# Optimization experiments

Measured on AMD Instinct MI355X. Metric: run time of the kernel, lower is better.

## Reference

```python
import jax, jax.numpy as jnp
import numpy as np

CDIM = 32
SCALES = (1, 16, 64, 256, 1024, 4096)  # last entry == T
INV_TEMP = 100.0
ENT_W = 0.1
COMMIT_W = 0.2
Q_SCALE = 1.0 / float(np.sqrt(CDIM))


def _interp_area(x, pt):
    # x: [B, T, C] -> [B, pt, C]; T divisible by pt so 'area' == block mean
    B, T, C = x.shape
    return x.reshape(B, pt, T // pt, C).mean(axis=2)


def _interp_linear(x, T):
    # x: [B, pt, C] -> [B, T, C]; mode='linear', align_corners=False
    pt = x.shape[1]
    pos = (jnp.arange(T, dtype=jnp.float32) + 0.5) * (pt / T) - 0.5
    pos = jnp.clip(pos, 0.0, pt - 1.0)
    lo = jnp.floor(pos).astype(jnp.int32)
    hi = jnp.minimum(lo + 1, pt - 1)
    w = (pos - lo.astype(jnp.float32))[None, :, None]
    return x[:, lo] * (1.0 - w) + x[:, hi] * w


def _bsq(f):
    # L2 normalize (torch F.normalize: clamp_min on norm)
    f = f / jnp.maximum(jnp.linalg.norm(f, axis=-1, keepdims=True), 1e-12)
    # sign quantize with STE
    zhat = jnp.where(f > 0, Q_SCALE, -Q_SCALE).astype(f.dtype)
    quantized = f + jax.lax.stop_gradient(zhat - f)
    # soft entropy loss
    p = jax.nn.sigmoid(-4.0 * f * (INV_TEMP / float(np.sqrt(CDIM))))
    prob = jnp.stack([p, 1.0 - p], axis=-1)  # [B, T, C, 2]
    ent = lambda c: -(c * jnp.log(c + 1e-8)).sum(axis=-1)
    per_sample_entropy = ent(prob).sum(axis=-1).mean()
    avg_prob = prob.mean(axis=(0, 1))  # [C, 2]
    cb_entropy = ent(avg_prob).sum()
    entropy_penalty = (per_sample_entropy - cb_entropy) / INV_TEMP
    commit = ((jax.lax.stop_gradient(quantized) - f) ** 2).sum(axis=-1).mean()
    aux = entropy_penalty * ENT_W + commit * COMMIT_W
    bits = (quantized > 0).astype(jnp.int32)
    return quantized, bits, aux


def setup_inputs() -> dict:
    key = jax.random.key(0)
    B, T, C = 128, SCALES[-1], CDIM
    return {"f_BTC": jax.random.normal(key, (B, T, C), dtype=jnp.float32)}


def reference(f_BTC):
    B, T, C = f_BTC.shape
    quantized_out = jnp.zeros_like(f_BTC)
    residual = f_BTC
    losses, bit_list = [], []
    for pt in SCALES:
        interp_res = _interp_area(residual, pt) if pt != T else residual
        q, bits, loss = _bsq(interp_res)
        q = _interp_linear(q, T) if pt != T else q
        residual = residual - jax.lax.stop_gradient(q)
        quantized_out = quantized_out + q
        bit_list.append(bits)
        losses.append(loss)
    all_losses = jnp.stack(losses, axis=-1)       # [num_scales]
    all_bits = jnp.concatenate(bit_list, axis=1)  # [B, sum(SCALES), C]
    return quantized_out, all_bits, all_losses
```

## Files before the change

kernel.cpp:

```cpp
#include <hip/hip_runtime.h>
#include <hip/hip_bf16.h>
#include <cstddef>
#include <cstdint>

#define NB 128
#define NT 4096
#define NC 32
#define BITROWS 5457
#define QV_ROWS 1361
#define QOUT_ELEMS (NB*NT*NC)
#define BITS_ELEMS (NB*BITROWS*NC)

#define ACC_OFF  22298624

__device__ __constant__ float kQSC = 0.17677669529663687f;
__device__ __constant__ float kSIG = 17.67766952966369f;

__device__ __forceinline__ float interp_eval(const float* __restrict__ q, int P, int t, int c) {
  float pos = ((float)t + 0.5f) * ((float)P * (1.0f / 4096.0f)) - 0.5f;
  pos = fminf(fmaxf(pos, 0.0f), (float)(P - 1));
  const int lo = (int)pos;
  const int hi = min(lo + 1, P - 1);
  const float w = pos - (float)lo;
  const float a = __fmul_rn(q[lo * NC + c], 1.0f - w);
  const float b = __fmul_rn(q[hi * NC + c], w);
  return __fadd_rn(a, b);
}

__device__ __forceinline__ float interp_slice(const float* __restrict__ q, int P, int base, int t, int c) {
  float pos = ((float)t + 0.5f) * ((float)P * (1.0f / 4096.0f)) - 0.5f;
  pos = fminf(fmaxf(pos, 0.0f), (float)(P - 1));
  const int lo = (int)pos;
  const int hi = min(lo + 1, P - 1);
  const float w = pos - (float)lo;
  const float a = __fmul_rn(q[(lo - base) * NC + c], 1.0f - w);
  const float b = __fmul_rn(q[(hi - base) * NC + c], w);
  return __fadd_rn(a, b);
}

__device__ __forceinline__ void process_elem(
    float msum, float invn, int b, int rowOff, int j, int c,
    float* qlsRow, float* __restrict__ qvG, float* __restrict__ bitsG,
    float& entA, float& comA, float& pA)
{
  const float m = msum * invn;
  float ss = m * m;
  #pragma unroll
  for (int mk = 16; mk; mk >>= 1) ss += __shfl_xor(ss, mk, 32);
  const float den = fmaxf(sqrtf(ss), 1e-12f);
  const float fn = m / den;
  const bool bit = fn > 0.0f;
  const float zh = bit ? kQSC : -kQSC;
  const float qvv = fn + (zh - fn);
  if (qlsRow) qlsRow[c] = qvv;
  if (qvG) qvG[(size_t)b * (QV_ROWS * NC) + (size_t)(rowOff + j) * NC + c] = qvv;
  bitsG[(size_t)b * (BITROWS * NC) + (size_t)(rowOff + j) * NC + c] = bit ? 1.0f : 0.0f;
  const float arg = (-4.0f * fn) * kSIG;
  const float p = 1.0f / (1.0f + __expf(-arg));
  const float ent = -(p * __logf(p + 1e-8f) + (1.0f - p) * __logf((1.0f - p) + 1e-8f));
  const float d = qvv - fn;
  entA += ent; comA += d * d; pA += p;
}

__device__ __forceinline__ void reduce_losses(
    int sIdx, float entA, float comA, float pA, int tid, int nWaves,
    double* __restrict__ acc, float* redE, float* redC, float* redP)
{
  float e = entA, cm = comA;
  #pragma unroll
  for (int mk = 32; mk; mk >>= 1) { e += __shfl_xor(e, mk, 64); cm += __shfl_xor(cm, mk, 64); }
  const float p = pA + __shfl_xor(pA, 32, 64);
  const int w = tid >> 6, lane = tid & 63;
  if (lane == 0) { redE[w] = e; redC[w] = cm; }
  if (lane < 32) redP[w * 32 + lane] = p;
  __syncthreads();
  if (tid == 0) {
    double te = 0.0, tc = 0.0;
    for (int i = 0; i < nWaves; ++i) { te += (double)redE[i]; tc += (double)redC[i]; }
    atomicAdd(&acc[sIdx], te);
    atomicAdd(&acc[6 + sIdx], tc);
  }
  if (tid < 32) {
    float tp = 0.0f;
    for (int i = 0; i < nWaves; ++i) tp += redP[i * 32 + tid];
    atomicAdd(&acc[12 + sIdx * 32 + tid], (double)tp);
  }
  __syncthreads();
}

__global__ __launch_bounds__(1024) void k_coarse(
    const float* __restrict__ f, float* __restrict__ qv,
    float* __restrict__ bitsOut, double* __restrict__ acc)
{
  __shared__ float S[256 * NC];
  __shared__ float qls[81 * NC];
  __shared__ float red[1024];
  __shared__ float redE[16], redC[16], redP[16 * 32];
  const int b = blockIdx.x, tid = threadIdx.x;
  const int c = tid & 31;

  for (int e = tid; e < 256 * NC; e += 1024) {
    const int cc = e & 31;
    const int j = e >> 5;
    const float* p = f + (size_t)b * (NT * NC) + (size_t)j * 16 * NC + cc;
    float s = 0.0f;
    #pragma unroll
    for (int k = 0; k < 16; ++k) s += p[k * NC];
    S[e] = s;
  }
  __syncthreads();

  float entA, comA, pA;

  entA = comA = pA = 0.0f;
  {
    const int g = tid >> 5;
    float part = 0.0f;
    #pragma unroll
    for (int j = 0; j < 8; ++j) part += S[(g * 8 + j) * NC + c];
    red[tid] = part;
  }
  __syncthreads();
  if (tid < 32) {
    float msum = 0.0f;
    for (int g = 0; g < 32; ++g) msum += red[g * 32 + tid];
    process_elem(msum, 1.0f / 4096.0f, b, 0, 0, tid, &qls[0], qv, bitsOut, entA, comA, pA);
  }
  reduce_losses(0, entA, comA, pA, tid, 16, acc, redE, redC, redP);
  {
    const float corr = 16.0f * qls[c];
    for (int e = tid; e < 8192; e += 1024) S[e] -= corr;
  }
  __syncthreads();

  entA = comA = pA = 0.0f;
  if (tid < 512) {
    const int j = tid >> 5;
    float msum = 0.0f;
    for (int jj = 0; jj < 16; ++jj) msum += S[(j * 16 + jj) * NC + c];
    process_elem(msum, 1.0f / 256.0f, b, 1, j, c, &qls[(1 + j) * NC], qv, bitsOut, entA, comA, pA);
  }
  reduce_losses(1, entA, comA, pA, tid, 16, acc, redE, redC, redP);
  for (int e = tid; e < 8192; e += 1024) {
    const int jj = e >> 5;
    float cs = 0.0f;
    #pragma unroll
    for (int k = 0; k < 16; ++k) cs += interp_eval(&qls[1 * NC], 16, jj * 16 + k, c);
    S[e] -= cs;
  }
  __syncthreads();

  entA = comA = pA = 0.0f;
  for (int out = tid; out < 2048; out += 1024) {
    const int j = out >> 5;
    float msum = 0.0f;
    #pragma unroll
    for (int jj = 0; jj < 4; ++jj) msum += S[(j * 4 + jj) * NC + c];
    process_elem(msum, 1.0f / 64.0f, b, 17, j, c, &qls[(17 + j) * NC], qv, bitsOut, entA, comA, pA);
  }
  reduce_losses(2, entA, comA, pA, tid, 16, acc, redE, redC, redP);
  for (int e = tid; e < 8192; e += 1024) {
    const int jj = e >> 5;
    float cs = 0.0f;
    #pragma unroll
    for (int k = 0; k < 16; ++k) cs += interp_eval(&qls[17 * NC], 64, jj * 16 + k, c);
    S[e] -= cs;
  }
  __syncthreads();

  entA = comA = pA = 0.0f;
  for (int out = tid; out < 8192; out += 1024) {
    const int j = out >> 5;
    process_elem(S[out], 1.0f / 16.0f, b, 81, j, c, nullptr, qv, bitsOut, entA, comA, pA);
  }
  reduce_losses(3, entA, comA, pA, tid, 16, acc, redE, redC, redP);
}

__global__ __launch_bounds__(256) void k_s45(
    const float* __restrict__ f, const float* __restrict__ qv,
    float* __restrict__ qout, float* __restrict__ bitsOut, double* __restrict__ acc)
{
  __shared__ float ql0[NC];
  __shared__ float ql1[3 * NC];
  __shared__ float ql2[6 * NC];
  __shared__ float ql3[18 * NC];
  __shared__ float ql4[66 * NC];
  __shared__ float redE[4], redC[4], redP[4 * 32];
  const int b = blockIdx.x >> 4, seg = blockIdx.x & 15;
  const int tid = threadIdx.x, c = tid & 31, rloc = tid >> 5;
  const int t0 = seg * 256;
  const float* __restrict__ qb = qv + (size_t)b * (QV_ROWS * NC);
  const float* __restrict__ fb = f + (size_t)b * (NT * NC);
  const int b1 = seg - 1, b2 = 4 * seg - 1, b3 = 16 * seg - 1, b4 = 64 * seg - 1;
  if (tid < NC) ql0[tid] = qb[tid];
  for (int e = tid; e < 3 * NC; e += 256) {
    const int r = min(max(b1 + (e >> 5), 0), 15);
    ql1[e] = qb[(1 + r) * NC + (e & 31)];
  }
  for (int e = tid; e < 6 * NC; e += 256) {
    const int r = min(max(b2 + (e >> 5), 0), 63);
    ql2[e] = qb[(17 + r) * NC + (e & 31)];
  }
  for (int e = tid; e < 18 * NC; e += 256) {
    const int r = min(max(b3 + (e >> 5), 0), 255);
    ql3[e] = qb[(81 + r) * NC + (e & 31)];
  }
  __syncthreads();

  float entA = 0.0f, comA = 0.0f, pA = 0.0f;
  for (int pass = 0; pass < 8; ++pass) {
    const int i = seg * 64 + pass * 8 + rloc;
    const float* fp = fb + (size_t)i * 4 * NC + c;
    float msum = 0.0f;
    #pragma unroll
    for (int k = 0; k < 4; ++k) {
      const int t = i * 4 + k;
      float r = fp[k * NC];
      r -= ql0[c];
      r -= interp_slice(ql1, 16,  b1, t, c);
      r -= interp_slice(ql2, 64,  b2, t, c);
      r -= interp_slice(ql3, 256, b3, t, c);
      msum += r;
    }
    process_elem(msum, 0.25f, b, 337, i, c,
                 &ql4[(size_t)(i - b4) * NC], nullptr, bitsOut, entA, comA, pA);
  }
  {
    int hr = -1;
    if (rloc == 0 && seg > 0)       hr = 64 * seg - 1;
    else if (rloc == 1 && seg < 15) hr = 64 * seg + 64;
    if (hr >= 0) {
      const float* fp = fb + (size_t)hr * 4 * NC + c;
      float msum = 0.0f;
      #pragma unroll
      for (int k = 0; k < 4; ++k) {
        const int t = hr * 4 + k;
        float r = fp[k * NC];
        r -= ql0[c];
        r -= interp_slice(ql1, 16,  b1, t, c);
        r -= interp_slice(ql2, 64,  b2, t, c);
        r -= interp_slice(ql3, 256, b3, t, c);
        msum += r;
      }
      const float m = msum * 0.25f;
      float ss = m * m;
      #pragma unroll
      for (int mk = 16; mk; mk >>= 1) ss += __shfl_xor(ss, mk, 32);
      const float den = fmaxf(sqrtf(ss), 1e-12f);
      const float fn = m / den;
      const float zh = (fn > 0.0f) ? kQSC : -kQSC;
      ql4[(size_t)(hr - b4) * NC + c] = fn + (zh - fn);
    }
  }
  reduce_losses(4, entA, comA, pA, tid, 4, acc, redE, redC, redP);

  entA = 0.0f; comA = 0.0f; pA = 0.0f;
  for (int pass = 0; pass < 32; ++pass) {
    const int t = t0 + pass * 8 + rloc;
    const float fv = fb[(size_t)t * NC + c];
    const float q0 = ql0[c];
    const float q1 = interp_slice(ql1, 16,   b1, t, c);
    const float q2 = interp_slice(ql2, 64,   b2, t, c);
    const float q3 = interp_slice(ql3, 256,  b3, t, c);
    const float q4 = interp_slice(ql4, 1024, b4, t, c);
    float r = fv;
    r -= q0; r -= q1; r -= q2; r -= q3; r -= q4;
    float qs = q0; qs += q1; qs += q2; qs += q3; qs += q4;
    float ss = r * r;
    #pragma unroll
    for (int mk = 16; mk; mk >>= 1) ss += __shfl_xor(ss, mk, 32);
    const float den = fmaxf(sqrtf(ss), 1e-12f);
    const float fn = r / den;
    const bool bit = fn > 0.0f;
    const float zh = bit ? kQSC : -kQSC;
    const float qvv = fn + (zh - fn);
    qout[(size_t)b * (NT * NC) + (size_t)t * NC + c] = qs + qvv;
    bitsOut[(size_t)b * (BITROWS * NC) + (size_t)(1361 + t) * NC + c] = bit ? 1.0f : 0.0f;
    const float arg = (-4.0f * fn) * kSIG;
    const float p = 1.0f / (1.0f + __expf(-arg));
    entA += -(p * __logf(p + 1e-8f) + (1.0f - p) * __logf((1.0f - p) + 1e-8f));
    const float d = qvv - fn;
    comA += d * d;
    pA += p;
  }
  reduce_losses(5, entA, comA, pA, tid, 4, acc, redE, redC, redP);
}

__global__ void k_losses(const double* __restrict__ acc, float* __restrict__ out) {
  const int s = threadIdx.x;
  if (s >= 6) return;
  const int pts[6] = {1, 16, 64, 256, 1024, 4096};
  const double n = 128.0 * (double)pts[s];
  const double pse = acc[s] / n;
  const double commit = acc[6 + s] / n;
  double cbe = 0.0;
  for (int c = 0; c < 32; ++c) {
    const double ap = acc[12 + s * 32 + c] / n;
    cbe += -(ap * log(ap + 1e-8) + (1.0 - ap) * log((1.0 - ap) + 1e-8));
  }
  const double pen = (pse - cbe) / 100.0;
  out[s] = (float)(pen * 0.1 + commit * 0.2);
}

extern "C" void kernel_launch(void* const* d_in, const int* in_sizes, int n_in,
                              void* d_out, int out_size, void* d_ws, size_t ws_size,
                              hipStream_t stream) {
  const float* f = (const float*)d_in[0];
  float* qout = (float*)d_out;
  float* bitsOut = qout + QOUT_ELEMS;
  float* lossesOut = qout + (QOUT_ELEMS + BITS_ELEMS);
  float* qv = (float*)d_ws;
  double* acc = (double*)((char*)d_ws + ACC_OFF);

  hipMemsetAsync(acc, 0, 204 * sizeof(double), stream);
  k_coarse<<<NB, 1024, 0, stream>>>(f, qv, bitsOut, acc);
  k_s45<<<NB * 16, 256, 0, stream>>>(f, qv, qout, bitsOut, acc);
  k_losses<<<1, 64, 0, stream>>>(acc, lossesOut);
}
```

Measured before the change: 335.0 us.

## Split coarse-scale kernel into parallel block-sum, scale-0 and two-segment coarse kernels

The single per-batch coarse kernel (128 blocks) is split into three kernels. A grid-wide kernel computes the 16-row block sums into workspace, a small kernel handles scale 0, and a two-segment-per-batch kernel handles scales 1-3 using halo rows that are recomputed redundantly for the interpolation. The goal is to raise parallelism beyond 128 blocks on a many-CU GPU and to spread the heavy input-reading sum across many blocks. The cost is extra launches, a round trip of the intermediate sums through global memory, and duplicated halo work.

After: 335.0 us. No clear change (-0.0%).

```diff
diff --git a/kernel.cpp b/kernel.cpp
--- a/kernel.cpp
+++ b/kernel.cpp
@@ -12,6 +12,7 @@
 #define BITS_ELEMS (NB*BITROWS*NC)
 
 #define ACC_OFF  22298624
+#define S16_OFF  22302720
 
 __device__ __constant__ float kQSC = 0.17677669529663687f;
 __device__ __constant__ float kSIG = 17.67766952966369f;
@@ -88,90 +89,140 @@
   __syncthreads();
 }
 
-__global__ __launch_bounds__(1024) void k_coarse(
-    const float* __restrict__ f, float* __restrict__ qv,
+__global__ __launch_bounds__(256) void k_sum16(const float* __restrict__ f, float* __restrict__ S16) {
+  const int idx = blockIdx.x * 256 + threadIdx.x;
+  if (idx >= NB * 256 * NC) return;
+  const int c = idx & 31;
+  const int j = (idx >> 5) & 255;
+  const int b = idx >> 13;
+  const float* p = f + (size_t)b * (NT * NC) + (size_t)j * 16 * NC + c;
+  float s = 0.0f;
+  #pragma unroll
+  for (int k = 0; k < 16; ++k) s += p[k * NC];
+  S16[idx] = s;
+}
+
+__global__ __launch_bounds__(1024) void k_s0(
+    const float* __restrict__ S16g, float* __restrict__ qv,
     float* __restrict__ bitsOut, double* __restrict__ acc)
 {
-  __shared__ float S[256 * NC];
-  __shared__ float qls[81 * NC];
   __shared__ float red[1024];
   __shared__ float redE[16], redC[16], redP[16 * 32];
-  const int b = blockIdx.x, tid = threadIdx.x;
-  const int c = tid & 31;
-
-  for (int e = tid; e < 256 * NC; e += 1024) {
-    const int cc = e & 31;
-    const int j = e >> 5;
-    const float* p = f + (size_t)b * (NT * NC) + (size_t)j * 16 * NC + cc;
-    float s = 0.0f;
-    #pragma unroll
-    for (int k = 0; k < 16; ++k) s += p[k * NC];
-    S[e] = s;
-  }
-  __syncthreads();
-
-  float entA, comA, pA;
-
-  entA = comA = pA = 0.0f;
+  const int b = blockIdx.x, tid = threadIdx.x, c = tid & 31;
+  const float* __restrict__ sb = S16g + (size_t)b * 8192;
   {
     const int g = tid >> 5;
     float part = 0.0f;
     #pragma unroll
-    for (int j = 0; j < 8; ++j) part += S[(g * 8 + j) * NC + c];
+    for (int j = 0; j < 8; ++j) part += sb[(size_t)(g * 8 + j) * NC + c];
     red[tid] = part;
   }
   __syncthreads();
+  float entA = 0.0f, comA = 0.0f, pA = 0.0f;
   if (tid < 32) {
     float msum = 0.0f;
     for (int g = 0; g < 32; ++g) msum += red[g * 32 + tid];
-    process_elem(msum, 1.0f / 4096.0f, b, 0, 0, tid, &qls[0], qv, bitsOut, entA, comA, pA);
+    process_elem(msum, 1.0f / 4096.0f, b, 0, 0, tid, nullptr, qv, bitsOut, entA, comA, pA);
   }
   reduce_losses(0, entA, comA, pA, tid, 16, acc, redE, redC, redP);
+}
+
+__global__ __launch_bounds__(1024) void k_coarse2(
+    const float* __restrict__ S16g,
+    float* __restrict__ qv, float* __restrict__ bitsOut, double* __restrict__ acc)
+{
+  __shared__ float S[144 * NC];
+  __shared__ float q1s[10 * NC];
+  __shared__ float q2s[34 * NC];
+  __shared__ float redE[16], redC[16], redP[16 * 32];
+  const int b = blockIdx.x >> 1, seg = blockIdx.x & 1;
+  const int tid = threadIdx.x, c = tid & 31;
+  const int start = seg * 112;
+  const int base1 = 8 * seg - 1, base2 = 32 * seg - 1;
+  const float* __restrict__ sb = S16g + (size_t)b * 8192;
+  const float* __restrict__ qb = qv + (size_t)b * (QV_ROWS * NC);
+
+  for (int e = tid; e < 144 * NC; e += 1024)
+    S[e] = sb[(size_t)(start + (e >> 5)) * NC + (e & 31)];
+  __syncthreads();
+
+  const float corr = 16.0f * qb[c];
+  for (int e = tid; e < 144 * NC; e += 1024) S[e] -= corr;
+  __syncthreads();
+
+  float entA, comA, pA;
+
+  entA = comA = pA = 0.0f;
+  if (tid < 256) {
+    const int jl = tid >> 5;
+    const int j = 8 * seg + jl;
+    float msum = 0.0f;
+    for (int jj = 0; jj < 16; ++jj) msum += S[(j * 16 + jj - start) * NC + c];
+    process_elem(msum, 1.0f / 256.0f, b, 1, j, c, &q1s[(j - base1) * NC], qv, bitsOut, entA, comA, pA);
+  } else if (tid < 288) {
+    const int jh = seg ? 7 : 8;
+    float msum = 0.0f;
+    for (int jj = 0; jj < 16; ++jj) msum += S[(jh * 16 + jj - start) * NC + c];
+    const float m = msum * (1.0f / 256.0f);
+    float ss = m * m;
+    #pragma unroll
+    for (int mk = 16; mk; mk >>= 1) ss += __shfl_xor(ss, mk, 32);
+    const float den = fmaxf(sqrtf(ss), 1e-12f);
+    const float fn = m / den;
+    const float zh = (fn > 0.0f) ? kQSC : -kQSC;
+    q1s[(jh - base1) * NC + c] = fn + (zh - fn);
+  }
+  reduce_losses(1, entA, comA, pA, tid, 16, acc, redE, redC, redP);
+
   {
-    const float corr = 16.0f * qls[c];
-    for (int e = tid; e < 8192; e += 1024) S[e] -= corr;
+    const int gc0 = seg ? 124 : 0;
+    for (int e = tid; e < 132 * NC; e += 1024) {
+      const int g = gc0 + (e >> 5);
+      float cs = 0.0f;
+      #pragma unroll
+      for (int k = 0; k < 16; ++k) cs += interp_slice(q1s, 16, base1, g * 16 + k, c);
+      S[(g - start) * NC + c] -= cs;
+    }
   }
   __syncthreads();
 
   entA = comA = pA = 0.0f;
-  if (tid < 512) {
-    const int j = tid >> 5;
-    float msum = 0.0f;
-    for (int jj = 0; jj < 16; ++jj) msum += S[(j * 16 + jj) * NC + c];
-    process_elem(msum, 1.0f / 256.0f, b, 1, j, c, &qls[(1 + j) * NC], qv, bitsOut, entA, comA, pA);
-  }
-  reduce_losses(1, entA, comA, pA, tid, 16, acc, redE, redC, redP);
-  for (int e = tid; e < 8192; e += 1024) {
-    const int jj = e >> 5;
+  {
+    const int j2 = 32 * seg + (tid >> 5);
+    float msum = 0.0f;
+    #pragma unroll
+    for (int jj = 0; jj < 4; ++jj) msum += S[(j2 * 4 + jj - start) * NC + c];
+    process_elem(msum, 1.0f / 64.0f, b, 17, j2, c, &q2s[(j2 - base2) * NC], qv, bitsOut, entA, comA, pA);
+  }
+  if (tid < 32) {
+    const int j2h = seg ? 31 : 32;
+    float msum = 0.0f;
+    #pragma unroll
+    for (int jj = 0; jj < 4; ++jj) msum += S[(j2h * 4 + jj - start) * NC + c];
+    const float m = msum * (1.0f / 64.0f);
+    float ss = m * m;
+    #pragma unroll
+    for (int mk = 16; mk; mk >>= 1) ss += __shfl_xor(ss, mk, 32);
+    const float den = fmaxf(sqrtf(ss), 1e-12f);
+    const float fn = m / den;
+    const float zh = (fn > 0.0f) ? kQSC : -kQSC;
+    q2s[(j2h - base2) * NC + c] = fn + (zh - fn);
+  }
+  reduce_losses(2, entA, comA, pA, tid, 16, acc, redE, redC, redP);
+
+  for (int e = tid; e < 128 * NC; e += 1024) {
+    const int g = 128 * seg + (e >> 5);
     float cs = 0.0f;
     #pragma unroll
-    for (int k = 0; k < 16; ++k) cs += interp_eval(&qls[1 * NC], 16, jj * 16 + k, c);
-    S[e] -= cs;
+    for (int k = 0; k < 16; ++k) cs += interp_slice(q2s, 64, base2, g * 16 + k, c);
+    S[(g - start) * NC + c] -= cs;
   }
   __syncthreads();
 
   entA = comA = pA = 0.0f;
-  for (int out = tid; out < 2048; out += 1024) {
-    const int j = out >> 5;
-    float msum = 0.0f;
-    #pragma unroll
-    for (int jj = 0; jj < 4; ++jj) msum += S[(j * 4 + jj) * NC + c];
-    process_elem(msum, 1.0f / 64.0f, b, 17, j, c, &qls[(17 + j) * NC], qv, bitsOut, entA, comA, pA);
-  }
-  reduce_losses(2, entA, comA, pA, tid, 16, acc, redE, redC, redP);
-  for (int e = tid; e < 8192; e += 1024) {
-    const int jj = e >> 5;
-    float cs = 0.0f;
-    #pragma unroll
-    for (int k = 0; k < 16; ++k) cs += interp_eval(&qls[17 * NC], 64, jj * 16 + k, c);
-    S[e] -= cs;
-  }
-  __syncthreads();
-
-  entA = comA = pA = 0.0f;
-  for (int out = tid; out < 8192; out += 1024) {
-    const int j = out >> 5;
-    process_elem(S[out], 1.0f / 16.0f, b, 81, j, c, nullptr, qv, bitsOut, entA, comA, pA);
+  for (int out = tid; out < 128 * NC; out += 1024) {
+    const int g = 128 * seg + (out >> 5);
+    process_elem(S[(g - start) * NC + c], 1.0f / 16.0f, b, 81, g, c, nullptr, qv, bitsOut, entA, comA, pA);
   }
   reduce_losses(3, entA, comA, pA, tid, 16, acc, redE, redC, redP);
 }
@@ -311,9 +362,12 @@
   float* lossesOut = qout + (QOUT_ELEMS + BITS_ELEMS);
   float* qv = (float*)d_ws;
   double* acc = (double*)((char*)d_ws + ACC_OFF);
+  float* S16 = (float*)((char*)d_ws + S16_OFF);
 
   hipMemsetAsync(acc, 0, 204 * sizeof(double), stream);
-  k_coarse<<<NB, 1024, 0, stream>>>(f, qv, bitsOut, acc);
+  k_sum16<<<4096, 256, 0, stream>>>(f, S16);
+  k_s0<<<NB, 1024, 0, stream>>>(S16, qv, bitsOut, acc);
+  k_coarse2<<<NB * 2, 1024, 0, stream>>>(S16, qv, bitsOut, acc);
   k_s45<<<NB * 16, 256, 0, stream>>>(f, qv, qout, bitsOut, acc);
   k_losses<<<1, 64, 0, stream>>>(acc, lossesOut);
 }
```
